# Optimization experiments

Measured on AMD Instinct MI355X. Metric: run time of the kernel, lower is better.

The kernel has to match this reference:

```python
import jax, jax.numpy as jnp
import numpy as np

KFAC = 4
D = 400  # latent dim hard-coded in the original module
SPLIT = D // KFAC


def setup_inputs() -> dict:
    key = jax.random.key(0)
    ks = jax.random.split(key, 8)
    B, N = 256, 20000
    return {
        "recon_x": jax.random.normal(ks[0], (B, N), jnp.float32),
        "x": jax.random.uniform(ks[1], (B, N), jnp.float32),
        "mu": jax.random.normal(ks[2], (B, D), jnp.float32),
        "logvar": jax.random.normal(ks[3], (B, D), jnp.float32),
        "logits_text": jax.random.normal(ks[4], (B, N), jnp.float32),
        "logits_rec": jax.random.normal(ks[5], (B, N), jnp.float32),
        "prior_mu": jax.random.normal(ks[6], (B, D), jnp.float32),
        "prior_logvar": jax.random.normal(ks[7], (B, D), jnp.float32),
    }


def _bures_wasserstein(means1, covs1, means2, covs2):
    # covs: [B, D, D] dense (diagonal-valued) matrices, per original module
    mean_dist_sq = jnp.sum((means1 - means2) ** 2, axis=1)
    sqrt_covs1 = jnp.linalg.cholesky(covs1)
    product = jnp.einsum('bij,bjk,blk->bil', sqrt_covs1, covs2, sqrt_covs1)
    sqrt_middle = jnp.linalg.cholesky(product)
    tr_sqrt_mid = jnp.trace(sqrt_middle, axis1=-2, axis2=-1)
    tr1 = jnp.trace(covs1, axis1=-2, axis2=-1)
    tr2 = jnp.trace(covs2, axis1=-2, axis2=-1)
    return mean_dist_sq + tr1 + tr2 - 2.0 * tr_sqrt_mid


def reference(recon_x, x, mu, logvar, logits_text, logits_rec, prior_mu, prior_logvar):
    anneal = 1.0
    epsilon = 1.0

    BCE_merged = -jnp.mean(jnp.mean(jax.nn.log_softmax(recon_x, axis=1) * x, axis=-1))
    BCE_text = -jnp.mean(jnp.mean(jax.nn.log_softmax(logits_text, axis=1) * x, axis=-1))
    BCE_rec = -jnp.mean(jnp.mean(jax.nn.log_softmax(logits_rec, axis=1) * x, axis=-1))
    BCE = (BCE_merged + BCE_text + BCE_rec) / 3.0

    lv = logvar.reshape(-1, KFAC, SPLIT)
    KLD1 = -0.5 * jnp.mean(jnp.mean(1.0 + lv - jnp.exp(lv), axis=-1))
    plv = prior_logvar.reshape(-1, KFAC, SPLIT)
    KLD2 = -0.5 * jnp.mean(jnp.mean(1.0 + plv - jnp.exp(plv), axis=-1))

    sigma2 = jnp.exp(logvar.reshape(-1, D))
    sigma2_prior = jnp.exp(prior_logvar.reshape(-1, D))
    sigma2_diag = jax.vmap(jnp.diag)(sigma2)            # [B, D, D]
    sigma2_prior_diag = jax.vmap(jnp.diag)(sigma2_prior)

    wasserstein_loss = jnp.mean(_bures_wasserstein(mu, sigma2_diag, prior_mu, sigma2_prior_diag))

    l = BCE + anneal / 2.0 * (KLD1 + KLD2) + epsilon * wasserstein_loss
    return (l, BCE, wasserstein_loss, BCE_rec, BCE_text, BCE_merged)
```

## Files before the change

kernel.cpp:

```cpp
#include <hip/hip_runtime.h>
#include <math.h>

#define B 256
#define N 20000
#define D 400
#define NV4 (N / 4)
#define CHUNKS 8
#define CV4 (NV4 / CHUNKS)
#define DV4 ((B * D) / 4)
#define NROWBLK (B * CHUNKS)
#define NDBLK 64
#define DPART_OFF (NROWBLK * 8)

__global__ __launch_bounds__(256) void phaseA(
    const float* __restrict__ recon, const float* __restrict__ x,
    const float* __restrict__ lt, const float* __restrict__ lr,
    const float* __restrict__ mu, const float* __restrict__ lv,
    const float* __restrict__ pmu, const float* __restrict__ plv,
    float* __restrict__ ws)
{
    __shared__ float red[4][8];
    const int bid = blockIdx.x;
    const int tid = threadIdx.x;
    const int wave = tid >> 6;
    const int lane = tid & 63;

    if (bid < NROWBLK) {
        const int r = bid >> 3;
        const int c = bid & 7;
        const float4* xr = (const float4*)(x + (size_t)r * N);
        const float4* zm = (const float4*)(recon + (size_t)r * N);
        const float4* zt = (const float4*)(lt + (size_t)r * N);
        const float4* zr = (const float4*)(lr + (size_t)r * N);

        float se0 = 0.f, se1 = 0.f, se2 = 0.f;
        float d0 = 0.f, d1 = 0.f, d2 = 0.f, sx = 0.f;

        const int jend = (c + 1) * CV4;
        for (int j = c * CV4 + tid; j < jend; j += 256) {
            float4 xv = xr[j];
            float4 a = zm[j];
            float4 b = zt[j];
            float4 cc = zr[j];
            sx += (xv.x + xv.y) + (xv.z + xv.w);
            d0 += a.x * xv.x + a.y * xv.y + a.z * xv.z + a.w * xv.w;
            d1 += b.x * xv.x + b.y * xv.y + b.z * xv.z + b.w * xv.w;
            d2 += cc.x * xv.x + cc.y * xv.y + cc.z * xv.z + cc.w * xv.w;
            se0 += (__expf(a.x) + __expf(a.y)) + (__expf(a.z) + __expf(a.w));
            se1 += (__expf(b.x) + __expf(b.y)) + (__expf(b.z) + __expf(b.w));
            se2 += (__expf(cc.x) + __expf(cc.y)) + (__expf(cc.z) + __expf(cc.w));
        }

        for (int off = 32; off > 0; off >>= 1) {
            se0 += __shfl_down(se0, off);
            se1 += __shfl_down(se1, off);
            se2 += __shfl_down(se2, off);
            d0 += __shfl_down(d0, off);
            d1 += __shfl_down(d1, off);
            d2 += __shfl_down(d2, off);
            sx += __shfl_down(sx, off);
        }
        if (lane == 0) {
            red[wave][0] = se0; red[wave][1] = se1; red[wave][2] = se2;
            red[wave][3] = d0;  red[wave][4] = d1;  red[wave][5] = d2;
            red[wave][6] = sx;
        }
        __syncthreads();
        if (tid == 0) {
            for (int w = 1; w < 4; ++w) {
                se0 += red[w][0]; se1 += red[w][1]; se2 += red[w][2];
                d0 += red[w][3]; d1 += red[w][4]; d2 += red[w][5];
                sx += red[w][6];
            }
            float4* slot = (float4*)(ws + (size_t)bid * 8);
            slot[0] = make_float4(se0, se1, se2, d0);
            slot[1] = make_float4(d1, d2, sx, 0.f);
        }
    } else {
        const int b2 = bid - NROWBLK;
        float k1 = 0.f, k2 = 0.f, wsm = 0.f;
        for (int j = b2 * 256 + tid; j < DV4; j += NDBLK * 256) {
            float4 v = ((const float4*)lv)[j];
            float4 p = ((const float4*)plv)[j];
            float4 a = ((const float4*)mu)[j];
            float4 q = ((const float4*)pmu)[j];

            k1 += (1.f + v.x - __expf(v.x)) + (1.f + v.y - __expf(v.y))
                + (1.f + v.z - __expf(v.z)) + (1.f + v.w - __expf(v.w));
            k2 += (1.f + p.x - __expf(p.x)) + (1.f + p.y - __expf(p.y))
                + (1.f + p.z - __expf(p.z)) + (1.f + p.w - __expf(p.w));

            float dm, ds;
            dm = a.x - q.x; ds = __expf(0.5f * v.x) - __expf(0.5f * p.x); wsm += dm * dm + ds * ds;
            dm = a.y - q.y; ds = __expf(0.5f * v.y) - __expf(0.5f * p.y); wsm += dm * dm + ds * ds;
            dm = a.z - q.z; ds = __expf(0.5f * v.z) - __expf(0.5f * p.z); wsm += dm * dm + ds * ds;
            dm = a.w - q.w; ds = __expf(0.5f * v.w) - __expf(0.5f * p.w); wsm += dm * dm + ds * ds;
        }

        for (int off = 32; off > 0; off >>= 1) {
            k1 += __shfl_down(k1, off);
            k2 += __shfl_down(k2, off);
            wsm += __shfl_down(wsm, off);
        }
        if (lane == 0) {
            red[wave][0] = k1; red[wave][1] = k2; red[wave][2] = wsm;
        }
        __syncthreads();
        if (tid == 0) {
            for (int w = 1; w < 4; ++w) {
                k1 += red[w][0]; k2 += red[w][1]; wsm += red[w][2];
            }
            float4* slot = (float4*)(ws + DPART_OFF + (size_t)b2 * 4);
            slot[0] = make_float4(k1, k2, wsm, 0.f);
        }
    }
}

__global__ __launch_bounds__(256) void phaseB(
    const float* __restrict__ ws, float* __restrict__ out)
{
    __shared__ float red[4][6];
    const int tid = threadIdx.x;
    const int wave = tid >> 6;
    const int lane = tid & 63;

    float se0 = 0.f, se1 = 0.f, se2 = 0.f;
    float d0 = 0.f, d1 = 0.f, d2 = 0.f, sx = 0.f;
    const float4* rp = (const float4*)(ws + (size_t)tid * 64);
    #pragma unroll
    for (int c = 0; c < 8; ++c) {
        float4 v0 = rp[2 * c];
        float4 v1 = rp[2 * c + 1];
        se0 += v0.x; se1 += v0.y; se2 += v0.z; d0 += v0.w;
        d1 += v1.x; d2 += v1.y; sx += v1.z;
    }
    float c0 = d0 - __logf(se0) * sx;
    float c1 = d1 - __logf(se1) * sx;
    float c2 = d2 - __logf(se2) * sx;

    float k1 = 0.f, k2 = 0.f, wsm = 0.f;
    if (tid < NDBLK) {
        float4 dp = ((const float4*)(ws + DPART_OFF))[tid];
        k1 = dp.x; k2 = dp.y; wsm = dp.z;
    }

    for (int off = 32; off > 0; off >>= 1) {
        c0 += __shfl_down(c0, off);
        c1 += __shfl_down(c1, off);
        c2 += __shfl_down(c2, off);
        k1 += __shfl_down(k1, off);
        k2 += __shfl_down(k2, off);
        wsm += __shfl_down(wsm, off);
    }
    if (lane == 0) {
        red[wave][0] = c0; red[wave][1] = c1; red[wave][2] = c2;
        red[wave][3] = k1; red[wave][4] = k2; red[wave][5] = wsm;
    }
    __syncthreads();
    if (tid == 0) {
        for (int w = 1; w < 4; ++w) {
            c0 += red[w][0]; c1 += red[w][1]; c2 += red[w][2];
            k1 += red[w][3]; k2 += red[w][4]; wsm += red[w][5];
        }
        const float invBN = 1.0f / ((float)B * (float)N);
        float bm = -c0 * invBN;
        float bt = -c1 * invBN;
        float br = -c2 * invBN;
        float bce = (bm + bt + br) * (1.0f / 3.0f);
        const float invBD = 1.0f / ((float)B * (float)D);
        float kld1 = -0.5f * k1 * invBD;
        float kld2 = -0.5f * k2 * invBD;
        float wass = wsm * (1.0f / (float)B);
        float l = bce + 0.5f * (kld1 + kld2) + wass;
        out[0] = l;
        out[1] = bce;
        out[2] = wass;
        out[3] = br;
        out[4] = bt;
        out[5] = bm;
    }
}

extern "C" void kernel_launch(void* const* d_in, const int* in_sizes, int n_in,
                              void* d_out, int out_size, void* d_ws, size_t ws_size,
                              hipStream_t stream)
{
    const float* recon = (const float*)d_in[0];
    const float* x     = (const float*)d_in[1];
    const float* mu    = (const float*)d_in[2];
    const float* lv    = (const float*)d_in[3];
    const float* lt    = (const float*)d_in[4];
    const float* lr    = (const float*)d_in[5];
    const float* pmu   = (const float*)d_in[6];
    const float* plv   = (const float*)d_in[7];
    float* out = (float*)d_out;
    float* ws  = (float*)d_ws;

    phaseA<<<NROWBLK + NDBLK, 256, 0, stream>>>(recon, x, lt, lr, mu, lv, pmu, plv, ws);
    phaseB<<<1, 256, 0, stream>>>(ws, out);
}
```

Baseline: 119.0 us.

## Fuse final reduction into main kernel via per-block flags and last-block spin-wait

Merges the two-kernel reduction into a single launch. Each producer block publishes its partial sums and then sets a per-block flag with a release store. The last block spin-waits on all flags and then performs the final combine. The latent-dimension blocks rise to 100 so each handles exactly one float4 per thread, and the last of them folds its own partials directly into the final reduction. This removes a kernel launch and the gap between kernels. The flags are never reset, so on repeated calls the waiting block can read stale partials from an earlier call, which is a race.

```diff
diff --git a/kernel.cpp b/kernel.cpp
--- a/kernel.cpp
+++ b/kernel.cpp
@@ -9,21 +9,26 @@
 #define CV4 (NV4 / CHUNKS)
 #define DV4 ((B * D) / 4)
 #define NROWBLK (B * CHUNKS)
-#define NDBLK 64
-#define DPART_OFF (NROWBLK * 8)
-
-__global__ __launch_bounds__(256) void phaseA(
+#define NDBLK 100
+#define NBLK (NROWBLK + NDBLK)
+#define NPROD (NBLK - 1)
+#define DPART_OFF 16384
+#define FLAG_OFF 24576
+#define MAGIC 0x5AD0F00Du
+
+__global__ __launch_bounds__(256) void fused(
     const float* __restrict__ recon, const float* __restrict__ x,
     const float* __restrict__ lt, const float* __restrict__ lr,
     const float* __restrict__ mu, const float* __restrict__ lv,
     const float* __restrict__ pmu, const float* __restrict__ plv,
-    float* __restrict__ ws)
+    float* __restrict__ ws, float* __restrict__ out)
 {
     __shared__ float red[4][8];
     const int bid = blockIdx.x;
     const int tid = threadIdx.x;
     const int wave = tid >> 6;
     const int lane = tid & 63;
+    unsigned* flags = (unsigned*)(ws + FLAG_OFF);
 
     if (bid < NROWBLK) {
         const int r = bid >> 3;
@@ -75,54 +80,64 @@
             float4* slot = (float4*)(ws + (size_t)bid * 8);
             slot[0] = make_float4(se0, se1, se2, d0);
             slot[1] = make_float4(d1, d2, sx, 0.f);
-        }
-    } else {
-        const int b2 = bid - NROWBLK;
-        float k1 = 0.f, k2 = 0.f, wsm = 0.f;
-        for (int j = b2 * 256 + tid; j < DV4; j += NDBLK * 256) {
-            float4 v = ((const float4*)lv)[j];
-            float4 p = ((const float4*)plv)[j];
-            float4 a = ((const float4*)mu)[j];
-            float4 q = ((const float4*)pmu)[j];
-
-            k1 += (1.f + v.x - __expf(v.x)) + (1.f + v.y - __expf(v.y))
-                + (1.f + v.z - __expf(v.z)) + (1.f + v.w - __expf(v.w));
-            k2 += (1.f + p.x - __expf(p.x)) + (1.f + p.y - __expf(p.y))
-                + (1.f + p.z - __expf(p.z)) + (1.f + p.w - __expf(p.w));
-
-            float dm, ds;
-            dm = a.x - q.x; ds = __expf(0.5f * v.x) - __expf(0.5f * p.x); wsm += dm * dm + ds * ds;
-            dm = a.y - q.y; ds = __expf(0.5f * v.y) - __expf(0.5f * p.y); wsm += dm * dm + ds * ds;
-            dm = a.z - q.z; ds = __expf(0.5f * v.z) - __expf(0.5f * p.z); wsm += dm * dm + ds * ds;
-            dm = a.w - q.w; ds = __expf(0.5f * v.w) - __expf(0.5f * p.w); wsm += dm * dm + ds * ds;
-        }
-
+            __hip_atomic_store(&flags[bid], MAGIC, __ATOMIC_RELEASE,
+                               __HIP_MEMORY_SCOPE_AGENT);
+        }
+        return;
+    }
+
+    const int b2 = bid - NROWBLK;
+    float k1 = 0.f, k2 = 0.f, wsm = 0.f;
+    {
+        const int j = b2 * 256 + tid;
+        float4 v = ((const float4*)lv)[j];
+        float4 p = ((const float4*)plv)[j];
+        float4 a = ((const float4*)mu)[j];
+        float4 q = ((const float4*)pmu)[j];
+
+        k1 = (1.f + v.x - __expf(v.x)) + (1.f + v.y - __expf(v.y))
+           + (1.f + v.z - __expf(v.z)) + (1.f + v.w - __expf(v.w));
+        k2 = (1.f + p.x - __expf(p.x)) + (1.f + p.y - __expf(p.y))
+           + (1.f + p.z - __expf(p.z)) + (1.f + p.w - __expf(p.w));
+
+        float dm, ds;
+        dm = a.x - q.x; ds = __expf(0.5f * v.x) - __expf(0.5f * p.x); wsm += dm * dm + ds * ds;
+        dm = a.y - q.y; ds = __expf(0.5f * v.y) - __expf(0.5f * p.y); wsm += dm * dm + ds * ds;
+        dm = a.z - q.z; ds = __expf(0.5f * v.z) - __expf(0.5f * p.z); wsm += dm * dm + ds * ds;
+        dm = a.w - q.w; ds = __expf(0.5f * v.w) - __expf(0.5f * p.w); wsm += dm * dm + ds * ds;
+    }
+
+    if (b2 < NDBLK - 1) {
+        float rk1 = k1, rk2 = k2, rws = wsm;
         for (int off = 32; off > 0; off >>= 1) {
-            k1 += __shfl_down(k1, off);
-            k2 += __shfl_down(k2, off);
-            wsm += __shfl_down(wsm, off);
+            rk1 += __shfl_down(rk1, off);
+            rk2 += __shfl_down(rk2, off);
+            rws += __shfl_down(rws, off);
         }
         if (lane == 0) {
-            red[wave][0] = k1; red[wave][1] = k2; red[wave][2] = wsm;
+            red[wave][0] = rk1; red[wave][1] = rk2; red[wave][2] = rws;
         }
         __syncthreads();
         if (tid == 0) {
             for (int w = 1; w < 4; ++w) {
-                k1 += red[w][0]; k2 += red[w][1]; wsm += red[w][2];
+                rk1 += red[w][0]; rk2 += red[w][1]; rws += red[w][2];
             }
             float4* slot = (float4*)(ws + DPART_OFF + (size_t)b2 * 4);
-            slot[0] = make_float4(k1, k2, wsm, 0.f);
-        }
-    }
-}
-
-__global__ __launch_bounds__(256) void phaseB(
-    const float* __restrict__ ws, float* __restrict__ out)
-{
-    __shared__ float red[4][6];
-    const int tid = threadIdx.x;
-    const int wave = tid >> 6;
-    const int lane = tid & 63;
+            slot[0] = make_float4(rk1, rk2, rws, 0.f);
+            __hip_atomic_store(&flags[bid], MAGIC, __ATOMIC_RELEASE,
+                               __HIP_MEMORY_SCOPE_AGENT);
+        }
+        return;
+    }
+
+    for (int j = tid; j < NPROD; j += 256) {
+        while (__hip_atomic_load(&flags[j], __ATOMIC_RELAXED,
+                                 __HIP_MEMORY_SCOPE_AGENT) != MAGIC) {
+            __builtin_amdgcn_s_sleep(2);
+        }
+    }
+    __syncthreads();
+    __threadfence();
 
     float se0 = 0.f, se1 = 0.f, se2 = 0.f;
     float d0 = 0.f, d1 = 0.f, d2 = 0.f, sx = 0.f;
@@ -138,10 +153,9 @@
     float c1 = d1 - __logf(se1) * sx;
     float c2 = d2 - __logf(se2) * sx;
 
-    float k1 = 0.f, k2 = 0.f, wsm = 0.f;
-    if (tid < NDBLK) {
+    if (tid < NDBLK - 1) {
         float4 dp = ((const float4*)(ws + DPART_OFF))[tid];
-        k1 = dp.x; k2 = dp.y; wsm = dp.z;
+        k1 += dp.x; k2 += dp.y; wsm += dp.z;
     }
 
     for (int off = 32; off > 0; off >>= 1) {
@@ -196,6 +210,5 @@
     float* out = (float*)d_out;
     float* ws  = (float*)d_ws;
 
-    phaseA<<<NROWBLK + NDBLK, 256, 0, stream>>>(recon, x, lt, lr, mu, lv, pmu, plv, ws);
-    phaseB<<<1, 256, 0, stream>>>(ws, out);
+    fused<<<NBLK, 256, 0, stream>>>(recon, x, lt, lr, mu, lv, pmu, plv, ws, out);
 }
```

Result: slower. 197.6 us (+66.1%).
